# Kernel optimization log

Measured on AMD Instinct MI355X. Metric: run time of the kernel, lower is better.

## Reference

```python
import jax, jax.numpy as jnp
import numpy as np

N, E, D_IN, D_OUT = 50000, 800000, 128, 128


def setup_inputs() -> dict:
    key = jax.random.key(0)
    ks = jax.random.split(key, 16)
    # edges with no self-loops (add_remaining_self_loops then simply appends one loop per node)
    row = jax.random.randint(ks[0], (E,), 0, N, dtype=jnp.int32)
    off = jax.random.randint(ks[1], (E,), 1, N, dtype=jnp.int32)
    col = (row + off) % N
    edge_index = jnp.stack([row, col], axis=0)
    s_in = 1.0 / np.sqrt(D_IN)
    s_out = 1.0 / np.sqrt(D_OUT)
    u = lambda k, shape, s: jax.random.uniform(k, shape, jnp.float32, -s, s)
    return {
        "x": jax.random.normal(ks[2], (N, D_IN), jnp.float32),
        "edge_index": edge_index,
        "W_hp": u(ks[3], (D_OUT, D_IN), s_in), "b_hp": u(ks[4], (D_OUT,), s_in),
        "W_lp": u(ks[5], (D_OUT, D_IN), s_in), "b_lp": u(ks[6], (D_OUT,), s_in),
        "W_i": u(ks[7], (D_OUT, D_IN), s_in), "b_i": u(ks[8], (D_OUT,), s_in),
        "wlin_h": u(ks[9], (D_OUT,), s_out), "blin_h": u(ks[10], (), s_out),
        "wlin_l": u(ks[11], (D_OUT,), s_out), "blin_l": u(ks[12], (), s_out),
        "wlin_i": u(ks[13], (D_OUT,), s_out), "blin_i": u(ks[14], (), s_out),
    }


def reference(x, edge_index, W_hp, b_hp, W_lp, b_lp, W_i, b_i,
              wlin_h, blin_h, wlin_l, blin_l, wlin_i, blin_i):
    n = x.shape[0]
    row, col = edge_index[0], edge_index[1]
    loop = jnp.arange(n, dtype=row.dtype)
    rf = jnp.concatenate([row, loop])  # sources incl. self-loops
    cf = jnp.concatenate([col, loop])  # targets incl. self-loops
    w = jnp.ones(rf.shape[0], x.dtype)
    # symmetric GCN normalization: D^{-1/2} A_hat D^{-1/2}
    deg = jax.ops.segment_sum(w, cf, num_segments=n)
    dinv = jnp.where(deg > 0, deg ** -0.5, 0.0).astype(x.dtype)
    w = dinv[rf] * w * dinv[cf]

    def agg(h):  # out[i] = sum_j w_e * h[j] over edges j->i
        return jax.ops.segment_sum(w[:, None] * h[rf], cf, num_segments=n)

    h_hp = x @ W_hp.T + b_hp
    H_hp = jax.nn.relu(h_hp - agg(h_hp))          # high-pass
    h_lp = x @ W_lp.T + b_lp
    H_lp = jax.nn.relu(agg(h_lp))                 # low-pass
    H_i = jax.nn.relu(x @ W_i.T + b_i)            # identity

    a_h = jax.nn.sigmoid(H_hp @ wlin_h + blin_h)  # [N]
    a_l = jax.nn.sigmoid(H_lp @ wlin_l + blin_l)
    a_i = jax.nn.sigmoid(H_i @ wlin_i + blin_i)
    # diag(alpha) @ H == alpha[:, None] * H
    return a_h[:, None] * H_hp + a_l[:, None] * H_lp + a_i[:, None] * H_i
```

## Files before the change

### kernel.cpp

```cpp
#include <hip/hip_runtime.h>
#include <cstdint>
#include <cstddef>

#define DEV __device__ __forceinline__

typedef __bf16 bf16x8 __attribute__((ext_vector_type(8)));
typedef float f32x4 __attribute__((ext_vector_type(4)));

DEV ushort f2b(float f) {
  uint u = __float_as_uint(f);
  return (ushort)((u + 0x7FFFu + ((u >> 16) & 1u)) >> 16);
}

DEV float4 shfl_xor4(float4 v, int m) {
  float4 r;
  r.x = __shfl_xor(v.x, m); r.y = __shfl_xor(v.y, m);
  r.z = __shfl_xor(v.z, m); r.w = __shfl_xor(v.w, m);
  return r;
}

DEV float4 unpack4(uint2 u) {
  float4 r;
  r.x = __uint_as_float(u.x << 16);
  r.y = __uint_as_float(u.x & 0xFFFF0000u);
  r.z = __uint_as_float(u.y << 16);
  r.w = __uint_as_float(u.y & 0xFFFF0000u);
  return r;
}

DEV void fma4(float4& a, float w, uint2 u) {
  float4 v = unpack4(u);
  a.x = fmaf(w, v.x, a.x); a.y = fmaf(w, v.y, a.y);
  a.z = fmaf(w, v.z, a.z); a.w = fmaf(w, v.w, a.w);
}

__global__ __launch_bounds__(256) void k_cvt_x(const float* __restrict__ x,
                                               ushort* __restrict__ xb, int n4) {
  int i = blockIdx.x * 256 + threadIdx.x;
  if (i >= n4) return;
  float4 v = ((const float4*)x)[i];
  ushort4 o; o.x = f2b(v.x); o.y = f2b(v.y); o.z = f2b(v.z); o.w = f2b(v.w);
  ((ushort4*)xb)[i] = o;
}

__global__ __launch_bounds__(256) void k_cvt_w(const float* __restrict__ W0,
                                               const float* __restrict__ W1,
                                               const float* __restrict__ W2,
                                               ushort* __restrict__ Wb) {
  const float* src = (blockIdx.x == 0) ? W0 : (blockIdx.x == 1) ? W1 : W2;
  ushort* dst = Wb + blockIdx.x * 16384;
  for (int i = threadIdx.x * 4; i < 16384; i += 1024) {
    float4 v = *(const float4*)(src + i);
    ushort4 o; o.x = f2b(v.x); o.y = f2b(v.y); o.z = f2b(v.z); o.w = f2b(v.w);
    *(ushort4*)(dst + i) = o;
  }
}

__global__ __launch_bounds__(256) void k_count(const int* __restrict__ col,
                                               int* __restrict__ cnt, int E) {
  int e = blockIdx.x * 256 + threadIdx.x;
  if (e < E) atomicAdd(&cnt[col[e]], 1);
}

__global__ __launch_bounds__(256) void k_blockscan(const int* __restrict__ cnt,
                                                   int* __restrict__ off,
                                                   float* __restrict__ dinv,
                                                   int* __restrict__ btot, int N) {
  __shared__ int ws[4];
  int t = threadIdx.x, lane = t & 63, wv = t >> 6;
  int i = blockIdx.x * 256 + t;
  int v = (i < N) ? cnt[i] : 0;
  int inc = v;
#pragma unroll
  for (int o = 1; o < 64; o <<= 1) {
    int u = __shfl_up(inc, o);
    if (lane >= o) inc += u;
  }
  if (lane == 63) ws[wv] = inc;
  __syncthreads();
  if (t == 0) {
    int s = 0;
#pragma unroll
    for (int w = 0; w < 4; ++w) { int tmp = ws[w]; ws[w] = s; s += tmp; }
  }
  __syncthreads();
  int excl = ws[wv] + inc - v;
  if (i < N) {
    off[i] = excl;
    dinv[i] = rsqrtf((float)v + 1.0f);
  }
  if (t == 255) btot[blockIdx.x] = excl + v;
}

__global__ __launch_bounds__(256) void k_scanb(const int* __restrict__ btot,
                                               int* __restrict__ bpre,
                                               int* __restrict__ off, int N, int NB) {
  __shared__ int ws[4];
  int t = threadIdx.x, lane = t & 63, wv = t >> 6;
  int v = (t < NB) ? btot[t] : 0;
  int inc = v;
#pragma unroll
  for (int o = 1; o < 64; o <<= 1) {
    int u = __shfl_up(inc, o);
    if (lane >= o) inc += u;
  }
  if (lane == 63) ws[wv] = inc;
  __syncthreads();
  if (t == 0) {
    int s = 0;
#pragma unroll
    for (int w = 0; w < 4; ++w) { int tmp = ws[w]; ws[w] = s; s += tmp; }
  }
  __syncthreads();
  int excl = ws[wv] + inc - v;
  if (t < NB) bpre[t] = excl;
  if (t == 255) off[N] = excl + v;
}

__global__ __launch_bounds__(256) void k_addoff(int* __restrict__ off,
                                                const int* __restrict__ bpre,
                                                int* __restrict__ cursor, int N) {
  int i = blockIdx.x * 256 + threadIdx.x;
  if (i < N) {
    int o = off[i] + bpre[blockIdx.x];
    off[i] = o;
    cursor[i] = o;
  }
}

__global__ __launch_bounds__(256) void k_scatter(const int* __restrict__ ei,
                                                 const float* __restrict__ dinv,
                                                 int* __restrict__ cursor,
                                                 int2* __restrict__ edata, int E) {
  int e = blockIdx.x * 256 + threadIdx.x;
  if (e >= E) return;
  int s = ei[e], d = ei[E + e];
  float w = dinv[s] * dinv[d];
  int p = atomicAdd(&cursor[d], 1);
  int2 v; v.x = s; v.y = __float_as_int(w);
  edata[p] = v;
}

__global__ __launch_bounds__(256, 2) void k_gemm_mfma(
    const ushort* __restrict__ xb, const ushort* __restrict__ Wb,
    const float* __restrict__ b_hp, const float* __restrict__ b_lp,
    const float* __restrict__ b_i,
    ushort* __restrict__ h_all, int N) {
  int m = blockIdx.y;
  const float* bias = (m == 0) ? b_hp : (m == 1) ? b_lp : b_i;
  int lane = (int)threadIdx.x & 63, wv = (int)threadIdx.x >> 6;
  int r = lane & 15, g = lane >> 4;

  const ushort* wp = Wb + m * 16384 + r * 128 + g * 8;
  bf16x8 Bf[8][4];
#pragma unroll
  for (int ct = 0; ct < 8; ++ct)
#pragma unroll
    for (int kc = 0; kc < 4; ++kc)
      Bf[ct][kc] = *(const bf16x8*)(const void*)(wp + ct * 2048 + kc * 32);

  float bv[8];
#pragma unroll
  for (int ct = 0; ct < 8; ++ct) bv[ct] = bias[ct * 16 + r];

  int NT = N >> 4;
  int stride = gridDim.x * 4;
  int t = blockIdx.x * 4 + wv;
  if (t >= NT) return;

  const ushort* ap0 = xb + r * 128 + g * 8;
  bf16x8 Af[4];
#pragma unroll
  for (int kc = 0; kc < 4; ++kc)
    Af[kc] = *(const bf16x8*)(const void*)(ap0 + (size_t)t * 2048 + kc * 32);

  while (t < NT) {
    int tn = t + stride;
    bf16x8 Afn[4];
    if (tn < NT) {
#pragma unroll
      for (int kc = 0; kc < 4; ++kc)
        Afn[kc] = *(const bf16x8*)(const void*)(ap0 + (size_t)tn * 2048 + kc * 32);
    }
    f32x4 acc[8];
#pragma unroll
    for (int ct = 0; ct < 8; ++ct) {
      f32x4 c; c[0] = bv[ct]; c[1] = bv[ct]; c[2] = bv[ct]; c[3] = bv[ct];
      acc[ct] = c;
    }
#pragma unroll
    for (int kc = 0; kc < 4; ++kc)
#pragma unroll
      for (int ct = 0; ct < 8; ++ct)
        acc[ct] = __builtin_amdgcn_mfma_f32_16x16x32_bf16(Af[kc], Bf[ct][kc], acc[ct], 0, 0, 0);

    ushort* op = h_all + (size_t)((t << 4) + g * 4) * 384 + m * 128 + r;
#pragma unroll
    for (int ct = 0; ct < 8; ++ct)
#pragma unroll
      for (int j = 0; j < 4; ++j) {
        float v = acc[ct][j];
        if (m == 2) v = fmaxf(v, 0.f);
        op[(size_t)j * 384 + ct * 16] = f2b(v);
      }
#pragma unroll
    for (int kc = 0; kc < 4; ++kc) Af[kc] = Afn[kc];
    t = tn;
  }
}

__global__ __launch_bounds__(256) void k_agg_final(
    const ushort* __restrict__ h_all, const float* __restrict__ dinv,
    const int* __restrict__ off, const int2* __restrict__ edata,
    const float* __restrict__ wlh, const float* __restrict__ wll,
    const float* __restrict__ wli,
    const float* __restrict__ pbh, const float* __restrict__ pbl,
    const float* __restrict__ pbi,
    float* __restrict__ out, int N) {
  int wv = __builtin_amdgcn_readfirstlane((int)threadIdx.x >> 6);
  int lane = (int)threadIdx.x & 63;
  int node = blockIdx.x * 4 + wv;
  if (node >= N) return;

  const ushort* hb = h_all + 4 * lane;
  int p0 = off[node], p1 = off[node + 1];

  float4 a0 = {0,0,0,0}, a1 = {0,0,0,0}, a2 = {0,0,0,0}, a3 = {0,0,0,0};
  int p = p0;
  for (; p + 4 <= p1; p += 4) {
    int2 e0 = edata[p], e1 = edata[p+1], e2 = edata[p+2], e3 = edata[p+3];
    uint2 u0 = *(const uint2*)(const void*)(hb + (size_t)e0.x * 384);
    uint2 u1 = *(const uint2*)(const void*)(hb + (size_t)e1.x * 384);
    uint2 u2 = *(const uint2*)(const void*)(hb + (size_t)e2.x * 384);
    uint2 u3 = *(const uint2*)(const void*)(hb + (size_t)e3.x * 384);
    fma4(a0, __int_as_float(e0.y), u0);
    fma4(a1, __int_as_float(e1.y), u1);
    fma4(a2, __int_as_float(e2.y), u2);
    fma4(a3, __int_as_float(e3.y), u3);
  }
  for (; p < p1; ++p) {
    int2 e = edata[p];
    uint2 u = *(const uint2*)(const void*)(hb + (size_t)e.x * 384);
    fma4(a0, __int_as_float(e.y), u);
  }
  float4 own;
  own.x = (a0.x + a1.x) + (a2.x + a3.x);
  own.y = (a0.y + a1.y) + (a2.y + a3.y);
  own.z = (a0.z + a1.z) + (a2.z + a3.z);
  own.w = (a0.w + a1.w) + (a2.w + a3.w);

  float di = dinv[node], wself = di * di;
  float4 sv = unpack4(*(const uint2*)(const void*)(hb + (size_t)node * 384));
  own.x = fmaf(wself, sv.x, own.x); own.y = fmaf(wself, sv.y, own.y);
  own.z = fmaf(wself, sv.z, own.z); own.w = fmaf(wself, sv.w, own.w);

  float4 oth = shfl_xor4(own, 32);
  float4 svo = shfl_xor4(sv, 32);
  bool hpside = (lane < 32);
  float4 hpSelf, aggHp, aggLp;
  hpSelf.x = hpside ? sv.x : svo.x; hpSelf.y = hpside ? sv.y : svo.y;
  hpSelf.z = hpside ? sv.z : svo.z; hpSelf.w = hpside ? sv.w : svo.w;
  aggHp.x = hpside ? own.x : oth.x; aggHp.y = hpside ? own.y : oth.y;
  aggHp.z = hpside ? own.z : oth.z; aggHp.w = hpside ? own.w : oth.w;
  aggLp.x = hpside ? oth.x : own.x; aggLp.y = hpside ? oth.y : own.y;
  aggLp.z = hpside ? oth.z : own.z; aggLp.w = hpside ? oth.w : own.w;

  float4 Hh, Hl;
  Hh.x = fmaxf(hpSelf.x - aggHp.x, 0.f); Hh.y = fmaxf(hpSelf.y - aggHp.y, 0.f);
  Hh.z = fmaxf(hpSelf.z - aggHp.z, 0.f); Hh.w = fmaxf(hpSelf.w - aggHp.w, 0.f);
  Hl.x = fmaxf(aggLp.x, 0.f); Hl.y = fmaxf(aggLp.y, 0.f);
  Hl.z = fmaxf(aggLp.z, 0.f); Hl.w = fmaxf(aggLp.w, 0.f);

  int c4 = 4 * (lane & 31);
  float4 hi4 = unpack4(*(const uint2*)(const void*)(h_all + (size_t)node * 384 + 256 + c4));
  float4 wh = *(const float4*)(wlh + c4);
  float4 wl = *(const float4*)(wll + c4);
  float4 wi = *(const float4*)(wli + c4);

  float dh = Hh.x * wh.x + Hh.y * wh.y + Hh.z * wh.z + Hh.w * wh.w;
  float dl = Hl.x * wl.x + Hl.y * wl.y + Hl.z * wl.z + Hl.w * wl.w;
  float dd = hi4.x * wi.x + hi4.y * wi.y + hi4.z * wi.z + hi4.w * wi.w;
#pragma unroll
  for (int o = 32; o > 0; o >>= 1) {
    dh += __shfl_xor(dh, o);
    dl += __shfl_xor(dl, o);
    dd += __shfl_xor(dd, o);
  }
  float a_h = 1.f / (1.f + __expf(-(0.5f * dh + pbh[0])));
  float a_l = 1.f / (1.f + __expf(-(0.5f * dl + pbl[0])));
  float a_i = 1.f / (1.f + __expf(-(0.5f * dd + pbi[0])));

  if (hpside) {
    float4 o4;
    o4.x = a_h * Hh.x + a_l * Hl.x + a_i * hi4.x;
    o4.y = a_h * Hh.y + a_l * Hl.y + a_i * hi4.y;
    o4.z = a_h * Hh.z + a_l * Hl.z + a_i * hi4.z;
    o4.w = a_h * Hh.w + a_l * Hl.w + a_i * hi4.w;
    *(float4*)(out + (size_t)node * 128 + c4) = o4;
  }
}

extern "C" void kernel_launch(void* const* d_in, const int* in_sizes, int n_in,
                              void* d_out, int out_size, void* d_ws, size_t ws_size,
                              hipStream_t stream) {
  const float* x     = (const float*)d_in[0];
  const int*   ei    = (const int*)d_in[1];
  const float* W_hp  = (const float*)d_in[2];
  const float* b_hp  = (const float*)d_in[3];
  const float* W_lp  = (const float*)d_in[4];
  const float* b_lp  = (const float*)d_in[5];
  const float* W_i   = (const float*)d_in[6];
  const float* b_i   = (const float*)d_in[7];
  const float* wlh   = (const float*)d_in[8];
  const float* pbh   = (const float*)d_in[9];
  const float* wll   = (const float*)d_in[10];
  const float* pbl   = (const float*)d_in[11];
  const float* wli   = (const float*)d_in[12];
  const float* pbi   = (const float*)d_in[13];
  float* out = (float*)d_out;

  int N = in_sizes[0] / 128;
  int E = in_sizes[1] / 2;
  int NB = (N + 255) / 256;

  ushort* xb    = (ushort*)d_ws;
  ushort* h_all = xb + (size_t)N * 128;
  ushort* Wb    = h_all + (size_t)N * 384;
  int2*   edata = (int2*)(Wb + 3 * 16384);
  float*  dinv  = (float*)(edata + E);
  int*    cnt   = (int*)(dinv + N);
  int*    off   = cnt + N;
  int*    cursor= off + N + 1;
  int*    btot  = cursor + N;
  int*    bpre  = btot + NB;

  hipMemsetAsync(cnt, 0, sizeof(int) * N, stream);
  k_cvt_x<<<(N * 128 / 4 + 255) / 256, 256, 0, stream>>>(x, xb, N * 128 / 4);
  k_cvt_w<<<3, 256, 0, stream>>>(W_hp, W_lp, W_i, Wb);
  k_count<<<(E + 255) / 256, 256, 0, stream>>>(ei + E, cnt, E);
  k_blockscan<<<NB, 256, 0, stream>>>(cnt, off, dinv, btot, N);
  k_scanb<<<1, 256, 0, stream>>>(btot, bpre, off, N, NB);
  k_addoff<<<NB, 256, 0, stream>>>(off, bpre, cursor, N);
  k_scatter<<<(E + 255) / 256, 256, 0, stream>>>(ei, dinv, cursor, edata, E);
  k_gemm_mfma<<<dim3(200, 3), 256, 0, stream>>>(xb, Wb, b_hp, b_lp, b_i, h_all, N);
  k_agg_final<<<(N + 3) / 4, 256, 0, stream>>>(
      h_all, dinv, off, edata, wlh, wll, wli, pbh, pbl, pbi, out, N);
}
```

Baseline: 278.1 us.

## Fuse graph preprocessing into one cooperative kernel and widen aggregation gathers

The memset, bf16 conversions, degree count, three scan stages and edge scatter are merged into one cooperative kernel with grid-wide syncs, replacing eight launches. The aggregation kernel now loads 16-byte bf16 rows, with the two half-waves taking alternate edges and combining their sums by shuffle, and writes output with nontemporal stores. The GEMM grid grows from 200 to 391 blocks in x. Grid syncs add their own barrier cost and need all 512 blocks resident at once.

```diff
diff --git a/kernel.cpp b/kernel.cpp
--- a/kernel.cpp
+++ b/kernel.cpp
@@ -1,6 +1,9 @@
 #include <hip/hip_runtime.h>
+#include <hip/hip_cooperative_groups.h>
 #include <cstdint>
 #include <cstddef>
+
+namespace cg = cooperative_groups;
 
 #define DEV __device__ __forceinline__
 
@@ -10,6 +13,11 @@
 DEV ushort f2b(float f) {
   uint u = __float_as_uint(f);
   return (ushort)((u + 0x7FFFu + ((u >> 16) & 1u)) >> 16);
+}
+
+DEV ushort4 cvt4(float4 v) {
+  ushort4 o; o.x = f2b(v.x); o.y = f2b(v.y); o.z = f2b(v.z); o.w = f2b(v.w);
+  return o;
 }
 
 DEV float4 shfl_xor4(float4 v, int m) {
@@ -19,126 +27,120 @@
   return r;
 }
 
-DEV float4 unpack4(uint2 u) {
-  float4 r;
-  r.x = __uint_as_float(u.x << 16);
-  r.y = __uint_as_float(u.x & 0xFFFF0000u);
-  r.z = __uint_as_float(u.y << 16);
-  r.w = __uint_as_float(u.y & 0xFFFF0000u);
-  return r;
-}
-
-DEV void fma4(float4& a, float w, uint2 u) {
-  float4 v = unpack4(u);
-  a.x = fmaf(w, v.x, a.x); a.y = fmaf(w, v.y, a.y);
-  a.z = fmaf(w, v.z, a.z); a.w = fmaf(w, v.w, a.w);
-}
-
-__global__ __launch_bounds__(256) void k_cvt_x(const float* __restrict__ x,
-                                               ushort* __restrict__ xb, int n4) {
-  int i = blockIdx.x * 256 + threadIdx.x;
-  if (i >= n4) return;
-  float4 v = ((const float4*)x)[i];
-  ushort4 o; o.x = f2b(v.x); o.y = f2b(v.y); o.z = f2b(v.z); o.w = f2b(v.w);
-  ((ushort4*)xb)[i] = o;
-}
-
-__global__ __launch_bounds__(256) void k_cvt_w(const float* __restrict__ W0,
-                                               const float* __restrict__ W1,
-                                               const float* __restrict__ W2,
-                                               ushort* __restrict__ Wb) {
-  const float* src = (blockIdx.x == 0) ? W0 : (blockIdx.x == 1) ? W1 : W2;
-  ushort* dst = Wb + blockIdx.x * 16384;
-  for (int i = threadIdx.x * 4; i < 16384; i += 1024) {
-    float4 v = *(const float4*)(src + i);
-    ushort4 o; o.x = f2b(v.x); o.y = f2b(v.y); o.z = f2b(v.z); o.w = f2b(v.w);
-    *(ushort4*)(dst + i) = o;
-  }
-}
-
-__global__ __launch_bounds__(256) void k_count(const int* __restrict__ col,
-                                               int* __restrict__ cnt, int E) {
-  int e = blockIdx.x * 256 + threadIdx.x;
-  if (e < E) atomicAdd(&cnt[col[e]], 1);
-}
-
-__global__ __launch_bounds__(256) void k_blockscan(const int* __restrict__ cnt,
-                                                   int* __restrict__ off,
-                                                   float* __restrict__ dinv,
-                                                   int* __restrict__ btot, int N) {
+DEV void unpack8(uint4 u, float4& lo, float4& hi) {
+  lo.x = __uint_as_float(u.x << 16);
+  lo.y = __uint_as_float(u.x & 0xFFFF0000u);
+  lo.z = __uint_as_float(u.y << 16);
+  lo.w = __uint_as_float(u.y & 0xFFFF0000u);
+  hi.x = __uint_as_float(u.z << 16);
+  hi.y = __uint_as_float(u.z & 0xFFFF0000u);
+  hi.z = __uint_as_float(u.w << 16);
+  hi.w = __uint_as_float(u.w & 0xFFFF0000u);
+}
+
+DEV void fma8(float4& alo, float4& ahi, float w, uint4 u) {
+  float4 lo, hi; unpack8(u, lo, hi);
+  alo.x = fmaf(w, lo.x, alo.x); alo.y = fmaf(w, lo.y, alo.y);
+  alo.z = fmaf(w, lo.z, alo.z); alo.w = fmaf(w, lo.w, alo.w);
+  ahi.x = fmaf(w, hi.x, ahi.x); ahi.y = fmaf(w, hi.y, ahi.y);
+  ahi.z = fmaf(w, hi.z, ahi.z); ahi.w = fmaf(w, hi.w, ahi.w);
+}
+
+__global__ __launch_bounds__(256) void k_coop_prep(
+    const float* x, ushort* xb,
+    const float* W0, const float* W1, const float* W2, ushort* Wb,
+    const int* ei, int2* edata, int* cnt, int* off, int* cursor,
+    float* dinv, int* btot, int* bpre, int N, int E) {
+  cg::grid_group grid = cg::this_grid();
+  int gsz = (int)gridDim.x * 256;
+  int gtid = (int)blockIdx.x * 256 + (int)threadIdx.x;
+  int t = threadIdx.x, ln = t & 63, wv = t >> 6;
   __shared__ int ws[4];
-  int t = threadIdx.x, lane = t & 63, wv = t >> 6;
-  int i = blockIdx.x * 256 + t;
-  int v = (i < N) ? cnt[i] : 0;
-  int inc = v;
-#pragma unroll
-  for (int o = 1; o < 64; o <<= 1) {
-    int u = __shfl_up(inc, o);
-    if (lane >= o) inc += u;
-  }
-  if (lane == 63) ws[wv] = inc;
-  __syncthreads();
-  if (t == 0) {
-    int s = 0;
-#pragma unroll
-    for (int w = 0; w < 4; ++w) { int tmp = ws[w]; ws[w] = s; s += tmp; }
-  }
-  __syncthreads();
-  int excl = ws[wv] + inc - v;
-  if (i < N) {
-    off[i] = excl;
-    dinv[i] = rsqrtf((float)v + 1.0f);
-  }
-  if (t == 255) btot[blockIdx.x] = excl + v;
-}
-
-__global__ __launch_bounds__(256) void k_scanb(const int* __restrict__ btot,
-                                               int* __restrict__ bpre,
-                                               int* __restrict__ off, int N, int NB) {
-  __shared__ int ws[4];
-  int t = threadIdx.x, lane = t & 63, wv = t >> 6;
-  int v = (t < NB) ? btot[t] : 0;
-  int inc = v;
-#pragma unroll
-  for (int o = 1; o < 64; o <<= 1) {
-    int u = __shfl_up(inc, o);
-    if (lane >= o) inc += u;
-  }
-  if (lane == 63) ws[wv] = inc;
-  __syncthreads();
-  if (t == 0) {
-    int s = 0;
-#pragma unroll
-    for (int w = 0; w < 4; ++w) { int tmp = ws[w]; ws[w] = s; s += tmp; }
-  }
-  __syncthreads();
-  int excl = ws[wv] + inc - v;
-  if (t < NB) bpre[t] = excl;
-  if (t == 255) off[N] = excl + v;
-}
-
-__global__ __launch_bounds__(256) void k_addoff(int* __restrict__ off,
-                                                const int* __restrict__ bpre,
-                                                int* __restrict__ cursor, int N) {
-  int i = blockIdx.x * 256 + threadIdx.x;
-  if (i < N) {
-    int o = off[i] + bpre[blockIdx.x];
-    off[i] = o;
-    cursor[i] = o;
-  }
-}
-
-__global__ __launch_bounds__(256) void k_scatter(const int* __restrict__ ei,
-                                                 const float* __restrict__ dinv,
-                                                 int* __restrict__ cursor,
-                                                 int2* __restrict__ edata, int E) {
-  int e = blockIdx.x * 256 + threadIdx.x;
-  if (e >= E) return;
-  int s = ei[e], d = ei[E + e];
-  float w = dinv[s] * dinv[d];
-  int p = atomicAdd(&cursor[d], 1);
-  int2 v; v.x = s; v.y = __float_as_int(w);
-  edata[p] = v;
+  int NB = (N + 255) / 256;
+
+  for (int i = gtid; i < N; i += gsz) cnt[i] = 0;
+  for (int i = gtid; i < 12288; i += gsz) {
+    int mi = i >> 12;
+    const float* src = (mi == 0) ? W0 : (mi == 1) ? W1 : W2;
+    int j = (i & 4095) << 2;
+    float4 v = *(const float4*)(src + j);
+    *(ushort4*)(Wb + ((size_t)i << 2)) = cvt4(v);
+  }
+  int n4 = N * 32;
+  for (int i = gtid; i < n4; i += gsz)
+    ((ushort4*)xb)[i] = cvt4(((const float4*)x)[i]);
+  grid.sync();
+
+  const int* col = ei + E;
+  for (int e = gtid; e < E; e += gsz) atomicAdd(&cnt[col[e]], 1);
+  grid.sync();
+
+  for (int c = blockIdx.x; c < NB; c += gridDim.x) {
+    int i = c * 256 + t;
+    int v = (i < N) ? cnt[i] : 0;
+    int inc = v;
+#pragma unroll
+    for (int o = 1; o < 64; o <<= 1) {
+      int u = __shfl_up(inc, o);
+      if (ln >= o) inc += u;
+    }
+    if (ln == 63) ws[wv] = inc;
+    __syncthreads();
+    if (t == 0) {
+      int s = 0;
+#pragma unroll
+      for (int w = 0; w < 4; ++w) { int tmp = ws[w]; ws[w] = s; s += tmp; }
+    }
+    __syncthreads();
+    int excl = ws[wv] + inc - v;
+    if (i < N) {
+      off[i] = excl;
+      dinv[i] = rsqrtf((float)v + 1.0f);
+    }
+    if (t == 255) btot[c] = excl + v;
+    __syncthreads();
+  }
+  grid.sync();
+
+  if (blockIdx.x == 0) {
+    int v = (t < NB) ? btot[t] : 0;
+    int inc = v;
+#pragma unroll
+    for (int o = 1; o < 64; o <<= 1) {
+      int u = __shfl_up(inc, o);
+      if (ln >= o) inc += u;
+    }
+    if (ln == 63) ws[wv] = inc;
+    __syncthreads();
+    if (t == 0) {
+      int s = 0;
+#pragma unroll
+      for (int w = 0; w < 4; ++w) { int tmp = ws[w]; ws[w] = s; s += tmp; }
+    }
+    __syncthreads();
+    int excl = ws[wv] + inc - v;
+    if (t < NB) bpre[t] = excl;
+    if (t == 255) off[N] = excl + v;
+  }
+  grid.sync();
+
+  for (int c = blockIdx.x; c < NB; c += gridDim.x) {
+    int i = c * 256 + t;
+    if (i < N) {
+      int o = off[i] + bpre[c];
+      off[i] = o;
+      cursor[i] = o;
+    }
+  }
+  grid.sync();
+
+  for (int e = gtid; e < E; e += gsz) {
+    int s = ei[e], d = col[e];
+    float w = dinv[s] * dinv[d];
+    int p = atomicAdd(&cursor[d], 1);
+    int2 v; v.x = s; v.y = __float_as_int(w);
+    edata[p] = v;
+  }
 }
 
 __global__ __launch_bounds__(256, 2) void k_gemm_mfma(
@@ -217,86 +219,112 @@
     const float* __restrict__ pbh, const float* __restrict__ pbl,
     const float* __restrict__ pbi,
     float* __restrict__ out, int N) {
-  int wv = __builtin_amdgcn_readfirstlane((int)threadIdx.x >> 6);
+  int wv = (int)threadIdx.x >> 6;
   int lane = (int)threadIdx.x & 63;
   int node = blockIdx.x * 4 + wv;
   if (node >= N) return;
-
-  const ushort* hb = h_all + 4 * lane;
+  int sl = lane & 31;
+  int half = lane >> 5;
+
+  const ushort* hb = h_all + sl * 8;
   int p0 = off[node], p1 = off[node + 1];
 
-  float4 a0 = {0,0,0,0}, a1 = {0,0,0,0}, a2 = {0,0,0,0}, a3 = {0,0,0,0};
-  int p = p0;
-  for (; p + 4 <= p1; p += 4) {
-    int2 e0 = edata[p], e1 = edata[p+1], e2 = edata[p+2], e3 = edata[p+3];
-    uint2 u0 = *(const uint2*)(const void*)(hb + (size_t)e0.x * 384);
-    uint2 u1 = *(const uint2*)(const void*)(hb + (size_t)e1.x * 384);
-    uint2 u2 = *(const uint2*)(const void*)(hb + (size_t)e2.x * 384);
-    uint2 u3 = *(const uint2*)(const void*)(hb + (size_t)e3.x * 384);
-    fma4(a0, __int_as_float(e0.y), u0);
-    fma4(a1, __int_as_float(e1.y), u1);
-    fma4(a2, __int_as_float(e2.y), u2);
-    fma4(a3, __int_as_float(e3.y), u3);
-  }
-  for (; p < p1; ++p) {
-    int2 e = edata[p];
-    uint2 u = *(const uint2*)(const void*)(hb + (size_t)e.x * 384);
-    fma4(a0, __int_as_float(e.y), u);
-  }
-  float4 own;
-  own.x = (a0.x + a1.x) + (a2.x + a3.x);
-  own.y = (a0.y + a1.y) + (a2.y + a3.y);
-  own.z = (a0.z + a1.z) + (a2.z + a3.z);
-  own.w = (a0.w + a1.w) + (a2.w + a3.w);
+  float4 a0l = {0,0,0,0}, a0h = {0,0,0,0}, a1l = {0,0,0,0}, a1h = {0,0,0,0};
+  float4 a2l = {0,0,0,0}, a2h = {0,0,0,0}, a3l = {0,0,0,0}, a3h = {0,0,0,0};
+
+  int p = p0 + half;
+  for (; p < p1 - 6; p += 8) {
+    int2 e0 = edata[p], e1 = edata[p + 2], e2 = edata[p + 4], e3 = edata[p + 6];
+    uint4 u0 = *(const uint4*)(const void*)(hb + (size_t)e0.x * 384);
+    uint4 u1 = *(const uint4*)(const void*)(hb + (size_t)e1.x * 384);
+    uint4 u2 = *(const uint4*)(const void*)(hb + (size_t)e2.x * 384);
+    uint4 u3 = *(const uint4*)(const void*)(hb + (size_t)e3.x * 384);
+    fma8(a0l, a0h, __int_as_float(e0.y), u0);
+    fma8(a1l, a1h, __int_as_float(e1.y), u1);
+    fma8(a2l, a2h, __int_as_float(e2.y), u2);
+    fma8(a3l, a3h, __int_as_float(e3.y), u3);
+  }
+  for (; p < p1; p += 2) {
+    int2 e0 = edata[p];
+    uint4 u0 = *(const uint4*)(const void*)(hb + (size_t)e0.x * 384);
+    fma8(a0l, a0h, __int_as_float(e0.y), u0);
+  }
+
+  float4 s_lo, s_hi;
+  s_lo.x = (a0l.x + a1l.x) + (a2l.x + a3l.x);
+  s_lo.y = (a0l.y + a1l.y) + (a2l.y + a3l.y);
+  s_lo.z = (a0l.z + a1l.z) + (a2l.z + a3l.z);
+  s_lo.w = (a0l.w + a1l.w) + (a2l.w + a3l.w);
+  s_hi.x = (a0h.x + a1h.x) + (a2h.x + a3h.x);
+  s_hi.y = (a0h.y + a1h.y) + (a2h.y + a3h.y);
+  s_hi.z = (a0h.z + a1h.z) + (a2h.z + a3h.z);
+  s_hi.w = (a0h.w + a1h.w) + (a2h.w + a3h.w);
+
+  float4 xlo = shfl_xor4(s_lo, 32), xhi = shfl_xor4(s_hi, 32);
+  s_lo.x += xlo.x; s_lo.y += xlo.y; s_lo.z += xlo.z; s_lo.w += xlo.w;
+  s_hi.x += xhi.x; s_hi.y += xhi.y; s_hi.z += xhi.z; s_hi.w += xhi.w;
 
   float di = dinv[node], wself = di * di;
-  float4 sv = unpack4(*(const uint2*)(const void*)(hb + (size_t)node * 384));
-  own.x = fmaf(wself, sv.x, own.x); own.y = fmaf(wself, sv.y, own.y);
-  own.z = fmaf(wself, sv.z, own.z); own.w = fmaf(wself, sv.w, own.w);
-
-  float4 oth = shfl_xor4(own, 32);
-  float4 svo = shfl_xor4(sv, 32);
-  bool hpside = (lane < 32);
-  float4 hpSelf, aggHp, aggLp;
-  hpSelf.x = hpside ? sv.x : svo.x; hpSelf.y = hpside ? sv.y : svo.y;
-  hpSelf.z = hpside ? sv.z : svo.z; hpSelf.w = hpside ? sv.w : svo.w;
-  aggHp.x = hpside ? own.x : oth.x; aggHp.y = hpside ? own.y : oth.y;
-  aggHp.z = hpside ? own.z : oth.z; aggHp.w = hpside ? own.w : oth.w;
-  aggLp.x = hpside ? oth.x : own.x; aggLp.y = hpside ? oth.y : own.y;
-  aggLp.z = hpside ? oth.z : own.z; aggLp.w = hpside ? oth.w : own.w;
-
-  float4 Hh, Hl;
-  Hh.x = fmaxf(hpSelf.x - aggHp.x, 0.f); Hh.y = fmaxf(hpSelf.y - aggHp.y, 0.f);
-  Hh.z = fmaxf(hpSelf.z - aggHp.z, 0.f); Hh.w = fmaxf(hpSelf.w - aggHp.w, 0.f);
-  Hl.x = fmaxf(aggLp.x, 0.f); Hl.y = fmaxf(aggLp.y, 0.f);
-  Hl.z = fmaxf(aggLp.z, 0.f); Hl.w = fmaxf(aggLp.w, 0.f);
-
-  int c4 = 4 * (lane & 31);
-  float4 hi4 = unpack4(*(const uint2*)(const void*)(h_all + (size_t)node * 384 + 256 + c4));
-  float4 wh = *(const float4*)(wlh + c4);
-  float4 wl = *(const float4*)(wll + c4);
-  float4 wi = *(const float4*)(wli + c4);
-
-  float dh = Hh.x * wh.x + Hh.y * wh.y + Hh.z * wh.z + Hh.w * wh.w;
-  float dl = Hl.x * wl.x + Hl.y * wl.y + Hl.z * wl.z + Hl.w * wl.w;
-  float dd = hi4.x * wi.x + hi4.y * wi.y + hi4.z * wi.z + hi4.w * wi.w;
-#pragma unroll
-  for (int o = 32; o > 0; o >>= 1) {
-    dh += __shfl_xor(dh, o);
-    dl += __shfl_xor(dl, o);
-    dd += __shfl_xor(dd, o);
-  }
-  float a_h = 1.f / (1.f + __expf(-(0.5f * dh + pbh[0])));
-  float a_l = 1.f / (1.f + __expf(-(0.5f * dl + pbl[0])));
-  float a_i = 1.f / (1.f + __expf(-(0.5f * dd + pbi[0])));
-
-  if (hpside) {
-    float4 o4;
-    o4.x = a_h * Hh.x + a_l * Hl.x + a_i * hi4.x;
-    o4.y = a_h * Hh.y + a_l * Hl.y + a_i * hi4.y;
-    o4.z = a_h * Hh.z + a_l * Hl.z + a_i * hi4.z;
-    o4.w = a_h * Hh.w + a_l * Hl.w + a_i * hi4.w;
-    *(float4*)(out + (size_t)node * 128 + c4) = o4;
+  uint4 su = *(const uint4*)(const void*)(h_all + (size_t)node * 384 + sl * 8);
+  float4 self_lo, self_hi; unpack8(su, self_lo, self_hi);
+  s_lo.x = fmaf(wself, self_lo.x, s_lo.x); s_lo.y = fmaf(wself, self_lo.y, s_lo.y);
+  s_lo.z = fmaf(wself, self_lo.z, s_lo.z); s_lo.w = fmaf(wself, self_lo.w, s_lo.w);
+  s_hi.x = fmaf(wself, self_hi.x, s_hi.x); s_hi.y = fmaf(wself, self_hi.y, s_hi.y);
+  s_hi.z = fmaf(wself, self_hi.z, s_hi.z); s_hi.w = fmaf(wself, self_hi.w, s_hi.w);
+
+  bool lpside = (sl >= 16);
+  float4 t_lo, t_hi;
+  t_lo.x = lpside ? fmaxf(s_lo.x, 0.f) : fmaxf(self_lo.x - s_lo.x, 0.f);
+  t_lo.y = lpside ? fmaxf(s_lo.y, 0.f) : fmaxf(self_lo.y - s_lo.y, 0.f);
+  t_lo.z = lpside ? fmaxf(s_lo.z, 0.f) : fmaxf(self_lo.z - s_lo.z, 0.f);
+  t_lo.w = lpside ? fmaxf(s_lo.w, 0.f) : fmaxf(self_lo.w - s_lo.w, 0.f);
+  t_hi.x = lpside ? fmaxf(s_hi.x, 0.f) : fmaxf(self_hi.x - s_hi.x, 0.f);
+  t_hi.y = lpside ? fmaxf(s_hi.y, 0.f) : fmaxf(self_hi.y - s_hi.y, 0.f);
+  t_hi.z = lpside ? fmaxf(s_hi.z, 0.f) : fmaxf(self_hi.z - s_hi.z, 0.f);
+  t_hi.w = lpside ? fmaxf(s_hi.w, 0.f) : fmaxf(self_hi.w - s_hi.w, 0.f);
+
+  float4 o_lo = shfl_xor4(t_lo, 16), o_hi = shfl_xor4(t_hi, 16);
+
+  int c0 = (sl & 15) * 8;
+  uint4 hu = *(const uint4*)(const void*)(h_all + (size_t)node * 384 + 256 + c0);
+  float4 hi_lo, hi_hi; unpack8(hu, hi_lo, hi_hi);
+
+  const float* wsel = lpside ? wll : wlh;
+  float4 w_lo = *(const float4*)(wsel + c0);
+  float4 w_hi = *(const float4*)(wsel + c0 + 4);
+  float4 wi_lo = *(const float4*)(wli + c0);
+  float4 wi_hi = *(const float4*)(wli + c0 + 4);
+
+  float dpart = t_lo.x * w_lo.x + t_lo.y * w_lo.y + t_lo.z * w_lo.z + t_lo.w * w_lo.w
+              + t_hi.x * w_hi.x + t_hi.y * w_hi.y + t_hi.z * w_hi.z + t_hi.w * w_hi.w;
+  float dipart = hi_lo.x * wi_lo.x + hi_lo.y * wi_lo.y + hi_lo.z * wi_lo.z + hi_lo.w * wi_lo.w
+               + hi_hi.x * wi_hi.x + hi_hi.y * wi_hi.y + hi_hi.z * wi_hi.z + hi_hi.w * wi_hi.w;
+#pragma unroll
+  for (int o = 1; o <= 8; o <<= 1) {
+    dpart += __shfl_xor(dpart, o);
+    dipart += __shfl_xor(dipart, o);
+  }
+  float dother = __shfl_xor(dpart, 16);
+  float dh = lpside ? dother : dpart;
+  float dl = lpside ? dpart : dother;
+
+  float a_h = 1.f / (1.f + __expf(-(dh + pbh[0])));
+  float a_l = 1.f / (1.f + __expf(-(dl + pbl[0])));
+  float a_i = 1.f / (1.f + __expf(-(dipart + pbi[0])));
+
+  if (lane < 16) {
+    f32x4 r_lo, r_hi;
+    r_lo[0] = a_h * t_lo.x + a_l * o_lo.x + a_i * hi_lo.x;
+    r_lo[1] = a_h * t_lo.y + a_l * o_lo.y + a_i * hi_lo.y;
+    r_lo[2] = a_h * t_lo.z + a_l * o_lo.z + a_i * hi_lo.z;
+    r_lo[3] = a_h * t_lo.w + a_l * o_lo.w + a_i * hi_lo.w;
+    r_hi[0] = a_h * t_hi.x + a_l * o_hi.x + a_i * hi_hi.x;
+    r_hi[1] = a_h * t_hi.y + a_l * o_hi.y + a_i * hi_hi.y;
+    r_hi[2] = a_h * t_hi.z + a_l * o_hi.z + a_i * hi_hi.z;
+    r_hi[3] = a_h * t_hi.w + a_l * o_hi.w + a_i * hi_hi.w;
+    f32x4* po = (f32x4*)(out + (size_t)node * 128 + c0);
+    __builtin_nontemporal_store(r_lo, po);
+    __builtin_nontemporal_store(r_hi, po + 1);
   }
 }
 
@@ -321,7 +349,6 @@
 
   int N = in_sizes[0] / 128;
   int E = in_sizes[1] / 2;
-  int NB = (N + 255) / 256;
 
   ushort* xb    = (ushort*)d_ws;
   ushort* h_all = xb + (size_t)N * 128;
@@ -332,17 +359,15 @@
   int*    off   = cnt + N;
   int*    cursor= off + N + 1;
   int*    btot  = cursor + N;
-  int*    bpre  = btot + NB;
-
-  hipMemsetAsync(cnt, 0, sizeof(int) * N, stream);
-  k_cvt_x<<<(N * 128 / 4 + 255) / 256, 256, 0, stream>>>(x, xb, N * 128 / 4);
-  k_cvt_w<<<3, 256, 0, stream>>>(W_hp, W_lp, W_i, Wb);
-  k_count<<<(E + 255) / 256, 256, 0, stream>>>(ei + E, cnt, E);
-  k_blockscan<<<NB, 256, 0, stream>>>(cnt, off, dinv, btot, N);
-  k_scanb<<<1, 256, 0, stream>>>(btot, bpre, off, N, NB);
-  k_addoff<<<NB, 256, 0, stream>>>(off, bpre, cursor, N);
-  k_scatter<<<(E + 255) / 256, 256, 0, stream>>>(ei, dinv, cursor, edata, E);
-  k_gemm_mfma<<<dim3(200, 3), 256, 0, stream>>>(xb, Wb, b_hp, b_lp, b_i, h_all, N);
+  int*    bpre  = btot + 256;
+
+  void* args[] = {(void*)&x, (void*)&xb, (void*)&W_hp, (void*)&W_lp, (void*)&W_i,
+                  (void*)&Wb, (void*)&ei, (void*)&edata, (void*)&cnt, (void*)&off,
+                  (void*)&cursor, (void*)&dinv, (void*)&btot, (void*)&bpre,
+                  (void*)&N, (void*)&E};
+  (void)hipLaunchCooperativeKernel((const void*)k_coop_prep, dim3(512), dim3(256),
+                                   args, 0, stream);
+  k_gemm_mfma<<<dim3(391, 3), 256, 0, stream>>>(xb, Wb, b_hp, b_lp, b_i, h_all, N);
   k_agg_final<<<(N + 3) / 4, 256, 0, stream>>>(
       h_all, dinv, off, edata, wlh, wll, wli, pbh, pbl, pbi, out, N);
 }
```

Result: slower. 594.5 us (+113.8%).

## Fuse x conversion into GEMM, merge small setup kernels, stage W in LDS

Applied to the files above, without the earlier changes.

The GEMM now reads fp32 x directly and converts it to bf16 in registers, so the separate x-conversion pass and its bf16 workspace copy go away. Each block computes all three projections for its row tiles, loading each bf16 weight matrix into swizzled shared memory in turn. The weight conversion is merged into the degree-count kernel, and the scan's second and third stages become one kernel that sets off[N]=E directly. This cuts launches and a full read/write of x, at the cost of loading weights into LDS per block and dropping the persistent-loop prefetch.

```diff
diff --git a/kernel.cpp b/kernel.cpp
--- a/kernel.cpp
+++ b/kernel.cpp
@@ -6,10 +6,16 @@
 
 typedef __bf16 bf16x8 __attribute__((ext_vector_type(8)));
 typedef float f32x4 __attribute__((ext_vector_type(4)));
+typedef unsigned short ushort8v __attribute__((ext_vector_type(8)));
 
 DEV ushort f2b(float f) {
   uint u = __float_as_uint(f);
   return (ushort)((u + 0x7FFFu + ((u >> 16) & 1u)) >> 16);
+}
+
+DEV ushort4 cvt4(float4 v) {
+  ushort4 o; o.x = f2b(v.x); o.y = f2b(v.y); o.z = f2b(v.z); o.w = f2b(v.w);
+  return o;
 }
 
 DEV float4 shfl_xor4(float4 v, int m) {
@@ -34,49 +40,38 @@
   a.z = fmaf(w, v.z, a.z); a.w = fmaf(w, v.w, a.w);
 }
 
-__global__ __launch_bounds__(256) void k_cvt_x(const float* __restrict__ x,
-                                               ushort* __restrict__ xb, int n4) {
-  int i = blockIdx.x * 256 + threadIdx.x;
-  if (i >= n4) return;
-  float4 v = ((const float4*)x)[i];
-  ushort4 o; o.x = f2b(v.x); o.y = f2b(v.y); o.z = f2b(v.z); o.w = f2b(v.w);
-  ((ushort4*)xb)[i] = o;
-}
-
-__global__ __launch_bounds__(256) void k_cvt_w(const float* __restrict__ W0,
-                                               const float* __restrict__ W1,
-                                               const float* __restrict__ W2,
-                                               ushort* __restrict__ Wb) {
-  const float* src = (blockIdx.x == 0) ? W0 : (blockIdx.x == 1) ? W1 : W2;
-  ushort* dst = Wb + blockIdx.x * 16384;
-  for (int i = threadIdx.x * 4; i < 16384; i += 1024) {
-    float4 v = *(const float4*)(src + i);
-    ushort4 o; o.x = f2b(v.x); o.y = f2b(v.y); o.z = f2b(v.z); o.w = f2b(v.w);
-    *(ushort4*)(dst + i) = o;
-  }
-}
-
-__global__ __launch_bounds__(256) void k_count(const int* __restrict__ col,
-                                               int* __restrict__ cnt, int E) {
-  int e = blockIdx.x * 256 + threadIdx.x;
+__global__ __launch_bounds__(256) void k_count_cvtw(
+    const int* __restrict__ col, int* __restrict__ cnt, int E, int nCB,
+    const float* __restrict__ W0, const float* __restrict__ W1,
+    const float* __restrict__ W2, ushort* __restrict__ Wb) {
+  int b = blockIdx.x;
+  if (b >= nCB) {
+    int mi = b - nCB;
+    const float* src = (mi == 0) ? W0 : (mi == 1) ? W1 : W2;
+    ushort* dst = Wb + mi * 16384;
+    for (int i = threadIdx.x * 4; i < 16384; i += 1024)
+      *(ushort4*)(dst + i) = cvt4(*(const float4*)(src + i));
+    return;
+  }
+  int e = b * 256 + threadIdx.x;
   if (e < E) atomicAdd(&cnt[col[e]], 1);
 }
 
-__global__ __launch_bounds__(256) void k_blockscan(const int* __restrict__ cnt,
-                                                   int* __restrict__ off,
-                                                   float* __restrict__ dinv,
-                                                   int* __restrict__ btot, int N) {
+__global__ __launch_bounds__(256) void k_scanA(const int* __restrict__ cnt,
+                                               int* __restrict__ off,
+                                               float* __restrict__ dinv,
+                                               int* __restrict__ btot, int N) {
   __shared__ int ws[4];
-  int t = threadIdx.x, lane = t & 63, wv = t >> 6;
+  int t = threadIdx.x, ln = t & 63, wv = t >> 6;
   int i = blockIdx.x * 256 + t;
   int v = (i < N) ? cnt[i] : 0;
   int inc = v;
 #pragma unroll
   for (int o = 1; o < 64; o <<= 1) {
     int u = __shfl_up(inc, o);
-    if (lane >= o) inc += u;
-  }
-  if (lane == 63) ws[wv] = inc;
+    if (ln >= o) inc += u;
+  }
+  if (ln == 63) ws[wv] = inc;
   __syncthreads();
   if (t == 0) {
     int s = 0;
@@ -92,19 +87,21 @@
   if (t == 255) btot[blockIdx.x] = excl + v;
 }
 
-__global__ __launch_bounds__(256) void k_scanb(const int* __restrict__ btot,
-                                               int* __restrict__ bpre,
-                                               int* __restrict__ off, int N, int NB) {
+__global__ __launch_bounds__(256) void k_scanBC(int* __restrict__ off,
+                                                const int* __restrict__ btot,
+                                                int* __restrict__ cursor,
+                                                int N, int E, int NB) {
   __shared__ int ws[4];
-  int t = threadIdx.x, lane = t & 63, wv = t >> 6;
+  __shared__ int pre_sh[256];
+  int t = threadIdx.x, ln = t & 63, wv = t >> 6;
   int v = (t < NB) ? btot[t] : 0;
   int inc = v;
 #pragma unroll
   for (int o = 1; o < 64; o <<= 1) {
     int u = __shfl_up(inc, o);
-    if (lane >= o) inc += u;
-  }
-  if (lane == 63) ws[wv] = inc;
+    if (ln >= o) inc += u;
+  }
+  if (ln == 63) ws[wv] = inc;
   __syncthreads();
   if (t == 0) {
     int s = 0;
@@ -112,20 +109,16 @@
     for (int w = 0; w < 4; ++w) { int tmp = ws[w]; ws[w] = s; s += tmp; }
   }
   __syncthreads();
-  int excl = ws[wv] + inc - v;
-  if (t < NB) bpre[t] = excl;
-  if (t == 255) off[N] = excl + v;
-}
-
-__global__ __launch_bounds__(256) void k_addoff(int* __restrict__ off,
-                                                const int* __restrict__ bpre,
-                                                int* __restrict__ cursor, int N) {
-  int i = blockIdx.x * 256 + threadIdx.x;
+  pre_sh[t] = ws[wv] + inc - v;
+  __syncthreads();
+  int bpre = pre_sh[blockIdx.x];
+  int i = blockIdx.x * 256 + t;
   if (i < N) {
-    int o = off[i] + bpre[blockIdx.x];
+    int o = off[i] + bpre;
     off[i] = o;
     cursor[i] = o;
   }
+  if (blockIdx.x == 0 && t == 0) off[N] = E;
 }
 
 __global__ __launch_bounds__(256) void k_scatter(const int* __restrict__ ei,
@@ -141,60 +134,61 @@
   edata[p] = v;
 }
 
-__global__ __launch_bounds__(256, 2) void k_gemm_mfma(
-    const ushort* __restrict__ xb, const ushort* __restrict__ Wb,
+__global__ __launch_bounds__(512) void k_gemm_fused(
+    const float* __restrict__ x, const ushort* __restrict__ Wb,
     const float* __restrict__ b_hp, const float* __restrict__ b_lp,
     const float* __restrict__ b_i,
     ushort* __restrict__ h_all, int N) {
-  int m = blockIdx.y;
-  const float* bias = (m == 0) ? b_hp : (m == 1) ? b_lp : b_i;
-  int lane = (int)threadIdx.x & 63, wv = (int)threadIdx.x >> 6;
+  __shared__ ushort Wl[16384];
+  int tid = (int)threadIdx.x, lane = tid & 63, wv = tid >> 6;
   int r = lane & 15, g = lane >> 4;
-
-  const ushort* wp = Wb + m * 16384 + r * 128 + g * 8;
-  bf16x8 Bf[8][4];
-#pragma unroll
-  for (int ct = 0; ct < 8; ++ct)
-#pragma unroll
-    for (int kc = 0; kc < 4; ++kc)
-      Bf[ct][kc] = *(const bf16x8*)(const void*)(wp + ct * 2048 + kc * 32);
-
-  float bv[8];
-#pragma unroll
-  for (int ct = 0; ct < 8; ++ct) bv[ct] = bias[ct * 16 + r];
-
   int NT = N >> 4;
-  int stride = gridDim.x * 4;
-  int t = blockIdx.x * 4 + wv;
-  if (t >= NT) return;
-
-  const ushort* ap0 = xb + r * 128 + g * 8;
+  int t = blockIdx.x * 8 + wv;
+  bool active = t < NT;
+
   bf16x8 Af[4];
-#pragma unroll
-  for (int kc = 0; kc < 4; ++kc)
-    Af[kc] = *(const bf16x8*)(const void*)(ap0 + (size_t)t * 2048 + kc * 32);
-
-  while (t < NT) {
-    int tn = t + stride;
-    bf16x8 Afn[4];
-    if (tn < NT) {
-#pragma unroll
-      for (int kc = 0; kc < 4; ++kc)
-        Afn[kc] = *(const bf16x8*)(const void*)(ap0 + (size_t)tn * 2048 + kc * 32);
+  if (active) {
+    const float* xp = x + ((size_t)t * 16 + r) * 128 + g * 8;
+#pragma unroll
+    for (int kc = 0; kc < 4; ++kc) {
+      float4 v0 = *(const float4*)(xp + kc * 32);
+      float4 v1 = *(const float4*)(xp + kc * 32 + 4);
+      ushort8v u;
+      u[0] = f2b(v0.x); u[1] = f2b(v0.y); u[2] = f2b(v0.z); u[3] = f2b(v0.w);
+      u[4] = f2b(v1.x); u[5] = f2b(v1.y); u[6] = f2b(v1.z); u[7] = f2b(v1.w);
+      Af[kc] = __builtin_bit_cast(bf16x8, u);
     }
+  }
+
+  for (int m = 0; m < 3; ++m) {
+    __syncthreads();
+    for (int i = tid; i < 2048; i += 512) {
+      int byte = i << 4;
+      int row = byte >> 8;
+      int swz = byte ^ ((row & 7) << 4);
+      *(ushort8v*)((char*)Wl + swz) = *(const ushort8v*)(Wb + m * 16384 + (i << 3));
+    }
+    __syncthreads();
+    if (!active) continue;
+    const float* bias = (m == 0) ? b_hp : (m == 1) ? b_lp : b_i;
     f32x4 acc[8];
 #pragma unroll
     for (int ct = 0; ct < 8; ++ct) {
-      f32x4 c; c[0] = bv[ct]; c[1] = bv[ct]; c[2] = bv[ct]; c[3] = bv[ct];
+      float bb = bias[ct * 16 + r];
+      f32x4 c; c[0] = bb; c[1] = bb; c[2] = bb; c[3] = bb;
       acc[ct] = c;
     }
 #pragma unroll
     for (int kc = 0; kc < 4; ++kc)
 #pragma unroll
-      for (int ct = 0; ct < 8; ++ct)
-        acc[ct] = __builtin_amdgcn_mfma_f32_16x16x32_bf16(Af[kc], Bf[ct][kc], acc[ct], 0, 0, 0);
-
-    ushort* op = h_all + (size_t)((t << 4) + g * 4) * 384 + m * 128 + r;
+      for (int ct = 0; ct < 8; ++ct) {
+        int row = ct * 16 + r;
+        int byte = row * 256 + kc * 64 + g * 16;
+        int swz = byte ^ ((row & 7) << 4);
+        bf16x8 B = *(const bf16x8*)((const char*)Wl + swz);
+        acc[ct] = __builtin_amdgcn_mfma_f32_16x16x32_bf16(Af[kc], B, acc[ct], 0, 0, 0);
+      }
+    ushort* op = h_all + (size_t)(t * 16 + g * 4) * 384 + m * 128 + r;
 #pragma unroll
     for (int ct = 0; ct < 8; ++ct)
 #pragma unroll
@@ -203,9 +197,6 @@
         if (m == 2) v = fmaxf(v, 0.f);
         op[(size_t)j * 384 + ct * 16] = f2b(v);
       }
-#pragma unroll
-    for (int kc = 0; kc < 4; ++kc) Af[kc] = Afn[kc];
-    t = tn;
   }
 }
 
@@ -217,7 +208,7 @@
     const float* __restrict__ pbh, const float* __restrict__ pbl,
     const float* __restrict__ pbi,
     float* __restrict__ out, int N) {
-  int wv = __builtin_amdgcn_readfirstlane((int)threadIdx.x >> 6);
+  int wv = (int)threadIdx.x >> 6;
   int lane = (int)threadIdx.x & 63;
   int node = blockIdx.x * 4 + wv;
   if (node >= N) return;
@@ -228,7 +219,7 @@
   float4 a0 = {0,0,0,0}, a1 = {0,0,0,0}, a2 = {0,0,0,0}, a3 = {0,0,0,0};
   int p = p0;
   for (; p + 4 <= p1; p += 4) {
-    int2 e0 = edata[p], e1 = edata[p+1], e2 = edata[p+2], e3 = edata[p+3];
+    int2 e0 = edata[p], e1 = edata[p + 1], e2 = edata[p + 2], e3 = edata[p + 3];
     uint2 u0 = *(const uint2*)(const void*)(hb + (size_t)e0.x * 384);
     uint2 u1 = *(const uint2*)(const void*)(hb + (size_t)e1.x * 384);
     uint2 u2 = *(const uint2*)(const void*)(hb + (size_t)e2.x * 384);
@@ -322,9 +313,9 @@
   int N = in_sizes[0] / 128;
   int E = in_sizes[1] / 2;
   int NB = (N + 255) / 256;
-
-  ushort* xb    = (ushort*)d_ws;
-  ushort* h_all = xb + (size_t)N * 128;
+  int nCB = (E + 255) / 256;
+
+  ushort* h_all = (ushort*)d_ws;
   ushort* Wb    = h_all + (size_t)N * 384;
   int2*   edata = (int2*)(Wb + 3 * 16384);
   float*  dinv  = (float*)(edata + E);
@@ -332,17 +323,13 @@
   int*    off   = cnt + N;
   int*    cursor= off + N + 1;
   int*    btot  = cursor + N;
-  int*    bpre  = btot + NB;
 
   hipMemsetAsync(cnt, 0, sizeof(int) * N, stream);
-  k_cvt_x<<<(N * 128 / 4 + 255) / 256, 256, 0, stream>>>(x, xb, N * 128 / 4);
-  k_cvt_w<<<3, 256, 0, stream>>>(W_hp, W_lp, W_i, Wb);
-  k_count<<<(E + 255) / 256, 256, 0, stream>>>(ei + E, cnt, E);
-  k_blockscan<<<NB, 256, 0, stream>>>(cnt, off, dinv, btot, N);
-  k_scanb<<<1, 256, 0, stream>>>(btot, bpre, off, N, NB);
-  k_addoff<<<NB, 256, 0, stream>>>(off, bpre, cursor, N);
+  k_count_cvtw<<<nCB + 3, 256, 0, stream>>>(ei + E, cnt, E, nCB, W_hp, W_lp, W_i, Wb);
+  k_scanA<<<NB, 256, 0, stream>>>(cnt, off, dinv, btot, N);
+  k_scanBC<<<NB, 256, 0, stream>>>(off, btot, cursor, N, E, NB);
   k_scatter<<<(E + 255) / 256, 256, 0, stream>>>(ei, dinv, cursor, edata, E);
-  k_gemm_mfma<<<dim3(200, 3), 256, 0, stream>>>(xb, Wb, b_hp, b_lp, b_i, h_all, N);
+  k_gemm_fused<<<(N / 16 + 7) / 8, 512, 0, stream>>>(x, Wb, b_hp, b_lp, b_i, h_all, N);
   k_agg_final<<<(N + 3) / 4, 256, 0, stream>>>(
       h_all, dinv, off, edata, wlh, wll, wli, pbh, pbl, pbi, out, N);
 }
```

Result: faster. 264.9 us (-4.7%).
